# Optimization experiments

Measured on AMD Instinct MI355X. Metric: run time of the kernel, lower is better.

## Reference

```python
import jax, jax.numpy as jnp
import numpy as np

N_NODES = 100000
N_EDGES = 3200000
N_GRAPHS = 1024
HID = 64


def setup_inputs() -> dict:
    key = jax.random.key(0)
    ks = jax.random.split(key, 10)
    x = jax.random.normal(ks[0], (N_NODES, 5), dtype=jnp.float32)
    edge_index = jax.random.randint(ks[1], (2, N_EDGES), 0, N_NODES, dtype=jnp.int64)
    batch = jnp.sort(jax.random.randint(ks[2], (N_NODES,), 0, N_GRAPHS, dtype=jnp.int64))
    s = 0.1
    return {
        "x": x,
        "edge_index": edge_index,
        "batch": batch,
        "W1a": jax.random.normal(ks[3], (5, HID), dtype=jnp.float32) * s,
        "b1a": jnp.zeros((HID,), jnp.float32),
        "W1b": jax.random.normal(ks[4], (HID, HID), dtype=jnp.float32) * s,
        "b1b": jnp.zeros((HID,), jnp.float32),
        "W2a": jax.random.normal(ks[5], (HID, HID), dtype=jnp.float32) * s,
        "b2a": jnp.zeros((HID,), jnp.float32),
        "W2b": jax.random.normal(ks[6], (HID, HID), dtype=jnp.float32) * s,
        "b2b": jnp.zeros((HID,), jnp.float32),
        "Wc": jax.random.normal(ks[7], (HID, 2), dtype=jnp.float32) * s,
        "bc": jnp.zeros((2,), jnp.float32),
    }


def _gin_conv(h, src, dst, Wa, ba, Wb, bb):
    # GINConv (eps=0): mlp(h + sum of neighbor messages), messages flow src -> dst
    agg = jax.ops.segment_sum(h[src], dst, num_segments=N_NODES)
    z = h + agg
    return jax.nn.relu(z @ Wa + ba) @ Wb + bb


def reference(x, edge_index, batch, W1a, b1a, W1b, b1b, W2a, b2a, W2b, b2b, Wc, bc):
    src, dst = edge_index[0], edge_index[1]
    h = jax.nn.relu(_gin_conv(x, src, dst, W1a, b1a, W1b, b1b))
    h = jax.nn.relu(_gin_conv(h, src, dst, W2a, b2a, W2b, b2b))
    # global_mean_pool over graphs
    sums = jax.ops.segment_sum(h, batch, num_segments=N_GRAPHS)        # [G, H]
    counts = jax.ops.segment_sum(jnp.ones((N_NODES, 1), h.dtype), batch,
                                 num_segments=N_GRAPHS)                 # [G, 1]
    pooled = sums / jnp.maximum(counts, 1.0)
    return pooled @ Wc + bc
```

## Files before the change

### kernel.cpp

```cpp
#include <hip/hip_runtime.h>

#define N_NODES   100000
#define N_EDGES   3200000
#define N_GRAPHS  1024
#define HID       64

#define NPB   128
#define NB    782
#define NBLK  512
#define EPB   (N_EDGES / NBLK)
#define CAP   6144

using bf16x8 = __attribute__((ext_vector_type(8))) short;
using f32x4  = __attribute__((ext_vector_type(4))) float;
using f16x4  = __attribute__((ext_vector_type(4))) _Float16;


__global__ void __launch_bounds__(512) k_p1(const int* __restrict__ dst,
                                            int* __restrict__ cnt) {
    __shared__ int h[NB];
    for (int i = threadIdx.x; i < NB; i += 512) h[i] = 0;
    __syncthreads();
    int base = blockIdx.x * EPB;
    for (int i = threadIdx.x; i < EPB; i += 512)
        atomicAdd(&h[dst[base + i] >> 7], 1);
    __syncthreads();
    for (int i = threadIdx.x; i < NB; i += 512)
        cnt[blockIdx.x * NB + i] = h[i];
}

__global__ void __launch_bounds__(512) k_p2(const int* __restrict__ cnt,
                                            int* __restrict__ excT,
                                            int* __restrict__ btot) {
    __shared__ int wsum[8];
    int b = blockIdx.x, t = threadIdx.x;
    int v = cnt[t * NB + b];
    int incl = v;
#pragma unroll
    for (int off = 1; off < 64; off <<= 1) {
        int u = __shfl_up(incl, off, 64);
        if ((t & 63) >= off) incl += u;
    }
    if ((t & 63) == 63) wsum[t >> 6] = incl;
    __syncthreads();
    int woff = 0;
    for (int w = 0; w < (t >> 6); ++w) woff += wsum[w];
    excT[b * NBLK + t] = woff + incl - v;
    if (t == 511) btot[b] = woff + incl;
}

__global__ void __launch_bounds__(1024) k_p2b(const int* __restrict__ btot,
                                              int* __restrict__ bbase,
                                              int* __restrict__ rp) {
    __shared__ int s[1024];
    int t = threadIdx.x;
    int v = (t < NB) ? btot[t] : 0;
    s[t] = v;
    __syncthreads();
    for (int off = 1; off < 1024; off <<= 1) {
        int u = (t >= off) ? s[t - off] : 0;
        __syncthreads();
        s[t] += u;
        __syncthreads();
    }
    if (t < NB) bbase[t] = s[t] - v;
    if (t == 0) { bbase[NB] = N_EDGES; rp[N_NODES] = N_EDGES; }
}

__global__ void __launch_bounds__(512) k_p3(const int* __restrict__ src,
                                            const int* __restrict__ dst,
                                            const int* __restrict__ excT,
                                            const int* __restrict__ bbase,
                                            unsigned int* __restrict__ packed) {
    __shared__ int cur[NB];
    int blk = blockIdx.x;
    for (int i = threadIdx.x; i < NB; i += 512)
        cur[i] = bbase[i] + excT[i * NBLK + blk];
    __syncthreads();
    int base = blk * EPB;
    for (int i = threadIdx.x; i < EPB; i += 512) {
        int d = dst[base + i];
        int pos = atomicAdd(&cur[d >> 7], 1);
        packed[pos] = ((unsigned)(d & 127) << 17) | (unsigned)src[base + i];
    }
}

__global__ void __launch_bounds__(512) k_p4(const unsigned int* __restrict__ packed,
                                            const int* __restrict__ bbase,
                                            int* __restrict__ rp,
                                            int* __restrict__ srcs) {
    __shared__ int hist[NPB + 1];
    __shared__ int stage[CAP];
    int b = blockIdx.x, t = threadIdx.x;
    int lo = bbase[b], hi = bbase[b + 1];
    int n_e = hi - lo;
    if (t < NPB + 1) hist[t] = 0;
    __syncthreads();
    for (int i = t; i < n_e; i += 512)
        atomicAdd(&hist[(packed[lo + i] >> 17) + 1], 1);
    __syncthreads();
    for (int off = 1; off < NPB + 1; off <<= 1) {
        int u = 0;
        if (t < NPB + 1 && t >= off) u = hist[t - off];
        __syncthreads();
        if (t < NPB + 1 && t >= off) hist[t] += u;
        __syncthreads();
    }
    int nbase = b * NPB;
    if (t < NPB && nbase + t < N_NODES) rp[nbase + t] = lo + hist[t];
    __syncthreads();
    if (n_e <= CAP) {
        for (int i = t; i < n_e; i += 512) {
            unsigned v = packed[lo + i];
            int pos = atomicAdd(&hist[v >> 17], 1);
            stage[pos] = (int)(v & 0x1FFFFu);
        }
        __syncthreads();
        for (int i = t; i < n_e; i += 512) srcs[lo + i] = stage[i];
    } else {
        for (int i = t; i < n_e; i += 512) {
            unsigned v = packed[lo + i];
            int pos = atomicAdd(&hist[v >> 17], 1);
            srcs[lo + pos] = (int)(v & 0x1FFFFu);
        }
    }
}


__global__ void __launch_bounds__(256) k_padb(
    const float* __restrict__ x, float* __restrict__ x8,
    const int* __restrict__ batch, int* __restrict__ gstart,
    int* __restrict__ gend) {
    int i = blockIdx.x * 256 + threadIdx.x;
    if (i < N_NODES * 8) {
        int n = i >> 3, j = i & 7;
        x8[i] = (j < 5) ? x[n * 5 + j] : 0.f;
    }
    if (i < N_NODES) {
        int g = batch[i];
        if (i == 0 || batch[i - 1] != g) atomicMin(&gstart[g], i);
        if (i == N_NODES - 1 || batch[i + 1] != g) atomicMax(&gend[g], i + 1);
    }
}


__global__ void k_wconv3(const float* __restrict__ Wa, const float* __restrict__ Wb,
                         const float* __restrict__ Wc_,
                         unsigned short* __restrict__ pa, unsigned short* __restrict__ pb,
                         unsigned short* __restrict__ pc) {
    int which = blockIdx.x >> 4;
    const float* W = (which == 0) ? Wa : (which == 1) ? Wb : Wc_;
    unsigned short* pack = (which == 0) ? pa : (which == 1) ? pb : pc;
    int i = (blockIdx.x & 15) * 256 + threadIdx.x;
    if (i >= 4096) return;
    int j    = i & 7;
    int lane = (i >> 3) & 63;
    int t    = (i >> 9) & 3;
    int ks   = (i >> 11) & 1;
    int k   = ks * 32 + (lane >> 4) * 8 + j;
    int col = t * 16 + (lane & 15);
    float w = W[k * HID + col];
    unsigned b = __float_as_uint(w);
    unsigned short hiw = (unsigned short)(b >> 16);
    float lf = w - __uint_as_float(b & 0xFFFF0000u);
    unsigned short low = (unsigned short)(__float_as_uint(lf) >> 16);
    pack[(((ks * 4 + t)) * 64 + lane) * 8 + j]   = hiw;
    pack[((8 + ks * 4 + t) * 64 + lane) * 8 + j] = low;
}

__device__ __forceinline__ void split8(const float* v, bf16x8& hi, bf16x8& lo) {
#pragma unroll
    for (int j = 0; j < 8; ++j) {
        unsigned b = __float_as_uint(v[j]);
        hi[j] = (short)(b >> 16);
        float lf = v[j] - __uint_as_float(b & 0xFFFF0000u);
        lo[j] = (short)(__float_as_uint(lf) >> 16);
    }
}


__global__ void __launch_bounds__(512) k_g1(
    const float* __restrict__ x8, const int* __restrict__ rp,
    const int* __restrict__ srcs, const float* __restrict__ W1a,
    const float* __restrict__ b1a, float* __restrict__ t1) {
    __shared__ float sWa[5 * HID];
    __shared__ float sba[HID];
    for (int i = threadIdx.x; i < 5 * HID; i += 512) sWa[i] = W1a[i];
    if (threadIdx.x < HID) sba[threadIdx.x] = b1a[threadIdx.x];
    __syncthreads();

    int wave = (blockIdx.x * 512 + threadIdx.x) >> 6;
    int lane = threadIdx.x & 63;
    int grp = lane >> 4, fq = lane & 15;
    int half = fq >> 3, f = fq & 7;
    int n = wave * 4 + grp;
    int e0 = rp[n], e1 = rp[n + 1];

    float a = 0.f;
    int e = e0;
    for (; e + 8 <= e1; e += 8) {
        int i0 = e + half;
        int s0 = srcs[i0], s1 = srcs[i0 + 2], s2 = srcs[i0 + 4], s3 = srcs[i0 + 6];
        float v0 = x8[(size_t)s0 * 8 + f];
        float v1 = x8[(size_t)s1 * 8 + f];
        float v2 = x8[(size_t)s2 * 8 + f];
        float v3 = x8[(size_t)s3 * 8 + f];
        a += (v0 + v1) + (v2 + v3);
    }
    for (; e < e1; e += 2) {
        int i = e + half;
        if (i < e1) a += x8[(size_t)srcs[i] * 8 + f];
    }
    a += __shfl_xor(a, 8, 16);

    float zf[5];
#pragma unroll
    for (int ff = 0; ff < 5; ++ff)
        zf[ff] = __shfl(a, ff, 16) + x8[(size_t)n * 8 + ff];

    float4 t = *reinterpret_cast<const float4*>(&sba[fq * 4]);
#pragma unroll
    for (int ff = 0; ff < 5; ++ff) {
        const float4 w = *reinterpret_cast<const float4*>(&sWa[ff * HID + fq * 4]);
        t.x += zf[ff] * w.x; t.y += zf[ff] * w.y;
        t.z += zf[ff] * w.z; t.w += zf[ff] * w.w;
    }
    t.x = fmaxf(t.x, 0.f); t.y = fmaxf(t.y, 0.f);
    t.z = fmaxf(t.z, 0.f); t.w = fmaxf(t.w, 0.f);
    *reinterpret_cast<float4*>(t1 + (size_t)n * HID + fq * 4) = t;
}


__global__ void __launch_bounds__(256) k_mm1(
    const float* __restrict__ t1, const unsigned short* __restrict__ packB,
    const float* __restrict__ bias, _Float16* __restrict__ h1h) {
    int wave = threadIdx.x >> 6, lane = threadIdx.x & 63;
    int q = lane >> 4;
    int n0 = blockIdx.x * 64 + wave * 16;
    int arow = n0 + (lane & 15);
    if (arow >= N_NODES) arow = N_NODES - 1;
    const float* ar = t1 + (size_t)arow * HID + q * 8;
    alignas(16) float a0[8], a1[8];
    *reinterpret_cast<float4*>(a0)     = *reinterpret_cast<const float4*>(ar);
    *reinterpret_cast<float4*>(a0 + 4) = *reinterpret_cast<const float4*>(ar + 4);
    *reinterpret_cast<float4*>(a1)     = *reinterpret_cast<const float4*>(ar + 32);
    *reinterpret_cast<float4*>(a1 + 4) = *reinterpret_cast<const float4*>(ar + 36);
    bf16x8 Ah0, Al0, Ah1, Al1;
    split8(a0, Ah0, Al0);
    split8(a1, Ah1, Al1);
    const bf16x8* bp = reinterpret_cast<const bf16x8*>(packB);
#pragma unroll
    for (int t = 0; t < 4; ++t) {
        bf16x8 Bh0 = bp[(t) * 64 + lane];
        bf16x8 Bh1 = bp[(4 + t) * 64 + lane];
        bf16x8 Bl0 = bp[(8 + t) * 64 + lane];
        bf16x8 Bl1 = bp[(12 + t) * 64 + lane];
        f32x4 acc = {0.f, 0.f, 0.f, 0.f};
        acc = __builtin_amdgcn_mfma_f32_16x16x32_bf16(Ah0, Bh0, acc, 0, 0, 0);
        acc = __builtin_amdgcn_mfma_f32_16x16x32_bf16(Ah1, Bh1, acc, 0, 0, 0);
        acc = __builtin_amdgcn_mfma_f32_16x16x32_bf16(Al0, Bh0, acc, 0, 0, 0);
        acc = __builtin_amdgcn_mfma_f32_16x16x32_bf16(Al1, Bh1, acc, 0, 0, 0);
        acc = __builtin_amdgcn_mfma_f32_16x16x32_bf16(Ah0, Bl0, acc, 0, 0, 0);
        acc = __builtin_amdgcn_mfma_f32_16x16x32_bf16(Ah1, Bl1, acc, 0, 0, 0);
        acc = __builtin_amdgcn_mfma_f32_16x16x32_bf16(Al0, Bl0, acc, 0, 0, 0);
        acc = __builtin_amdgcn_mfma_f32_16x16x32_bf16(Al1, Bl1, acc, 0, 0, 0);
        int col = (lane & 15) + 16 * t;
        float bv = bias[col];
#pragma unroll
        for (int r = 0; r < 4; ++r) {
            int node = n0 + q * 4 + r;
            if (node < N_NODES)
                h1h[(size_t)node * HID + col] = (_Float16)fmaxf(acc[r] + bv, 0.f);
        }
    }
}


__device__ __forceinline__ void acc4(float4& z, f16x4 r) {
    z.x += (float)r.x; z.y += (float)r.y; z.z += (float)r.z; z.w += (float)r.w;
}

__global__ void __launch_bounds__(512) k_g2(
    const _Float16* __restrict__ h1h, const int* __restrict__ rp,
    const int* __restrict__ srcs, float* __restrict__ z2) {
    int wave = (blockIdx.x * 512 + threadIdx.x) >> 6;
    int lane = threadIdx.x & 63;
    int grp = lane >> 4, fq = lane & 15;
    int n = wave * 4 + grp;
    int e0 = rp[n], e1 = rp[n + 1];

    const f16x4* __restrict__ H = reinterpret_cast<const f16x4*>(h1h);
    f16x4 rs = H[(size_t)n * 16 + fq];
    float4 z = {(float)rs.x, (float)rs.y, (float)rs.z, (float)rs.w};

    int e = e0;
    for (; e + 8 <= e1; e += 8) {
        int s0 = srcs[e],     s1 = srcs[e + 1], s2 = srcs[e + 2], s3 = srcs[e + 3];
        int s4 = srcs[e + 4], s5 = srcs[e + 5], s6 = srcs[e + 6], s7 = srcs[e + 7];
        f16x4 v0 = H[(size_t)s0 * 16 + fq];
        f16x4 v1 = H[(size_t)s1 * 16 + fq];
        f16x4 v2 = H[(size_t)s2 * 16 + fq];
        f16x4 v3 = H[(size_t)s3 * 16 + fq];
        f16x4 v4 = H[(size_t)s4 * 16 + fq];
        f16x4 v5 = H[(size_t)s5 * 16 + fq];
        f16x4 v6 = H[(size_t)s6 * 16 + fq];
        f16x4 v7 = H[(size_t)s7 * 16 + fq];
        acc4(z, v0); acc4(z, v1); acc4(z, v2); acc4(z, v3);
        acc4(z, v4); acc4(z, v5); acc4(z, v6); acc4(z, v7);
    }
    for (; e < e1; ++e) {
        f16x4 v = H[(size_t)srcs[e] * 16 + fq];
        acc4(z, v);
    }
    *reinterpret_cast<float4*>(z2 + (size_t)n * HID + fq * 4) = z;
}


__global__ void __launch_bounds__(256) k_mm2(
    const float* __restrict__ z2, const unsigned short* __restrict__ packA,
    const unsigned short* __restrict__ packB, const float* __restrict__ b2a,
    const float* __restrict__ b2b, float* __restrict__ u_out) {
    __shared__ __align__(16) float tm[4][16][68];
    int wave = threadIdx.x >> 6, lane = threadIdx.x & 63;
    int q = lane >> 4;
    int n0 = blockIdx.x * 64 + wave * 16;
    int arow = n0 + (lane & 15);
    if (arow >= N_NODES) arow = N_NODES - 1;

    {
        const float* ar = z2 + (size_t)arow * HID + q * 8;
        alignas(16) float a0[8], a1[8];
        *reinterpret_cast<float4*>(a0)     = *reinterpret_cast<const float4*>(ar);
        *reinterpret_cast<float4*>(a0 + 4) = *reinterpret_cast<const float4*>(ar + 4);
        *reinterpret_cast<float4*>(a1)     = *reinterpret_cast<const float4*>(ar + 32);
        *reinterpret_cast<float4*>(a1 + 4) = *reinterpret_cast<const float4*>(ar + 36);
        bf16x8 Ah0, Al0, Ah1, Al1;
        split8(a0, Ah0, Al0);
        split8(a1, Ah1, Al1);
        const bf16x8* bp = reinterpret_cast<const bf16x8*>(packA);
#pragma unroll
        for (int t = 0; t < 4; ++t) {
            bf16x8 Bh0 = bp[(t) * 64 + lane];
            bf16x8 Bh1 = bp[(4 + t) * 64 + lane];
            bf16x8 Bl0 = bp[(8 + t) * 64 + lane];
            bf16x8 Bl1 = bp[(12 + t) * 64 + lane];
            f32x4 acc = {0.f, 0.f, 0.f, 0.f};
            acc = __builtin_amdgcn_mfma_f32_16x16x32_bf16(Ah0, Bh0, acc, 0, 0, 0);
            acc = __builtin_amdgcn_mfma_f32_16x16x32_bf16(Ah1, Bh1, acc, 0, 0, 0);
            acc = __builtin_amdgcn_mfma_f32_16x16x32_bf16(Al0, Bh0, acc, 0, 0, 0);
            acc = __builtin_amdgcn_mfma_f32_16x16x32_bf16(Al1, Bh1, acc, 0, 0, 0);
            acc = __builtin_amdgcn_mfma_f32_16x16x32_bf16(Ah0, Bl0, acc, 0, 0, 0);
            acc = __builtin_amdgcn_mfma_f32_16x16x32_bf16(Ah1, Bl1, acc, 0, 0, 0);
            acc = __builtin_amdgcn_mfma_f32_16x16x32_bf16(Al0, Bl0, acc, 0, 0, 0);
            acc = __builtin_amdgcn_mfma_f32_16x16x32_bf16(Al1, Bl1, acc, 0, 0, 0);
            int col = (lane & 15) + 16 * t;
            float bv = b2a[col];
#pragma unroll
            for (int r = 0; r < 4; ++r)
                tm[wave][q * 4 + r][col] = fmaxf(acc[r] + bv, 0.f);
        }
    }

    const float* tr = &tm[wave][lane & 15][0];
    alignas(16) float c0[8], c1[8];
    *reinterpret_cast<float4*>(c0)     = *reinterpret_cast<const float4*>(tr + q * 8);
    *reinterpret_cast<float4*>(c0 + 4) = *reinterpret_cast<const float4*>(tr + q * 8 + 4);
    *reinterpret_cast<float4*>(c1)     = *reinterpret_cast<const float4*>(tr + 32 + q * 8);
    *reinterpret_cast<float4*>(c1 + 4) = *reinterpret_cast<const float4*>(tr + 36 + q * 8);
    bf16x8 Ch0, Cl0, Ch1, Cl1;
    split8(c0, Ch0, Cl0);
    split8(c1, Ch1, Cl1);

    const bf16x8* bp = reinterpret_cast<const bf16x8*>(packB);
#pragma unroll
    for (int t = 0; t < 4; ++t) {
        bf16x8 Bh0 = bp[(t) * 64 + lane];
        bf16x8 Bh1 = bp[(4 + t) * 64 + lane];
        bf16x8 Bl0 = bp[(8 + t) * 64 + lane];
        bf16x8 Bl1 = bp[(12 + t) * 64 + lane];
        f32x4 acc = {0.f, 0.f, 0.f, 0.f};
        acc = __builtin_amdgcn_mfma_f32_16x16x32_bf16(Ch0, Bh0, acc, 0, 0, 0);
        acc = __builtin_amdgcn_mfma_f32_16x16x32_bf16(Ch1, Bh1, acc, 0, 0, 0);
        acc = __builtin_amdgcn_mfma_f32_16x16x32_bf16(Cl0, Bh0, acc, 0, 0, 0);
        acc = __builtin_amdgcn_mfma_f32_16x16x32_bf16(Cl1, Bh1, acc, 0, 0, 0);
        acc = __builtin_amdgcn_mfma_f32_16x16x32_bf16(Ch0, Bl0, acc, 0, 0, 0);
        acc = __builtin_amdgcn_mfma_f32_16x16x32_bf16(Ch1, Bl1, acc, 0, 0, 0);
        acc = __builtin_amdgcn_mfma_f32_16x16x32_bf16(Cl0, Bl0, acc, 0, 0, 0);
        acc = __builtin_amdgcn_mfma_f32_16x16x32_bf16(Cl1, Bl1, acc, 0, 0, 0);
        int col = (lane & 15) + 16 * t;
        float bv = b2b[col];
#pragma unroll
        for (int r = 0; r < 4; ++r) {
            int node = n0 + q * 4 + r;
            if (node < N_NODES)
                u_out[(size_t)node * HID + col] = fmaxf(acc[r] + bv, 0.f);
        }
    }
}


__global__ void __launch_bounds__(256) k_final2(
    const float* __restrict__ u, const int* __restrict__ gstart,
    const int* __restrict__ gend, const float* __restrict__ Wc,
    const float* __restrict__ bc, float* __restrict__ out) {
    __shared__ float red[4][64];
    int g = blockIdx.x, t = threadIdx.x;
    int col = t & 63, ch = t >> 6;
    int s = gstart[g], e = gend[g];
    float acc = 0.f;
    for (int i = s + ch; i < e; i += 4)
        acc += u[(size_t)i * HID + col];
    red[ch][col] = acc;
    __syncthreads();
    if (t < 64) {
        float p = red[0][t] + red[1][t] + red[2][t] + red[3][t];
        float count = (float)(e - s);
        p /= fmaxf(count, 1.0f);
        float r0 = p * Wc[t * 2 + 0];
        float r1 = p * Wc[t * 2 + 1];
#pragma unroll
        for (int m = 1; m < 64; m <<= 1) {
            r0 += __shfl_xor(r0, m, 64);
            r1 += __shfl_xor(r1, m, 64);
        }
        if (t == 0) {
            out[g * 2 + 0] = r0 + bc[0];
            out[g * 2 + 1] = r1 + bc[1];
        }
    }
}


extern "C" void kernel_launch(void* const* d_in, const int* in_sizes, int n_in,
                              void* d_out, int out_size, void* d_ws, size_t ws_size,
                              hipStream_t stream) {
    const float* x   = (const float*)d_in[0];
    const int* ei    = (const int*)d_in[1];
    const int* batch = (const int*)d_in[2];
    const float* W1a = (const float*)d_in[3];
    const float* b1a = (const float*)d_in[4];
    const float* W1b = (const float*)d_in[5];
    const float* b1b = (const float*)d_in[6];
    const float* W2a = (const float*)d_in[7];
    const float* b2a = (const float*)d_in[8];
    const float* W2b = (const float*)d_in[9];
    const float* b2b = (const float*)d_in[10];
    const float* Wc  = (const float*)d_in[11];
    const float* bc  = (const float*)d_in[12];
    float* out = (float*)d_out;

    const int* src = ei;
    const int* dst = ei + N_EDGES;

    char* ws = (char*)d_ws;
    size_t off = 0;
    auto alloc = [&](size_t bytes) {
        char* p = ws + off;
        off += (bytes + 127) & ~size_t(127);
        return p;
    };
    int*   rp    = (int*)alloc((N_NODES + 1) * sizeof(int));
    int*   srcs  = (int*)alloc((size_t)N_EDGES * sizeof(int));
    _Float16* h1h = (_Float16*)alloc((size_t)N_NODES * HID * sizeof(_Float16));
    float* t1    = (float*)alloc((size_t)N_NODES * HID * sizeof(float));
    float* z2    = (float*)alloc((size_t)N_NODES * HID * sizeof(float));
    float* x8    = (float*)alloc((size_t)N_NODES * 8 * sizeof(float));
    int*   btot  = (int*)alloc(NB * sizeof(int));
    int*   bbase = (int*)alloc((NB + 1) * sizeof(int));
    int*   gstart= (int*)alloc(N_GRAPHS * sizeof(int));
    int*   gend  = (int*)alloc(N_GRAPHS * sizeof(int));
    unsigned short* pk1b = (unsigned short*)alloc(8192 * sizeof(unsigned short));
    unsigned short* pk2a = (unsigned short*)alloc(8192 * sizeof(unsigned short));
    unsigned short* pk2b = (unsigned short*)alloc(8192 * sizeof(unsigned short));

    int* bcnt = (int*)t1;
    int* excT = (int*)t1 + NBLK * NB;
    unsigned int* packed = (unsigned int*)z2;

    hipMemsetAsync(gstart, 0x7F, N_GRAPHS * sizeof(int), stream);
    hipMemsetAsync(gend, 0, N_GRAPHS * sizeof(int), stream);

    k_p1 <<<NBLK, 512, 0, stream>>>(dst, bcnt);
    k_padb<<<(N_NODES * 8) / 256, 256, 0, stream>>>(x, x8, batch, gstart, gend);
    k_wconv3<<<48, 256, 0, stream>>>(W1b, W2a, W2b, pk1b, pk2a, pk2b);
    k_p2 <<<NB, 512, 0, stream>>>(bcnt, excT, btot);
    k_p2b<<<1, 1024, 0, stream>>>(btot, bbase, rp);
    k_p3 <<<NBLK, 512, 0, stream>>>(src, dst, excT, bbase, packed);
    k_p4 <<<NB, 512, 0, stream>>>(packed, bbase, rp, srcs);

    int gblocks = N_NODES / 32;
    int mblocks = (N_NODES + 63) / 64;

    k_g1 <<<gblocks, 512, 0, stream>>>(x8, rp, srcs, W1a, b1a, t1);
    k_mm1<<<mblocks, 256, 0, stream>>>(t1, pk1b, b1b, h1h);
    k_g2 <<<gblocks, 512, 0, stream>>>(h1h, rp, srcs, z2);
    k_mm2<<<mblocks, 256, 0, stream>>>(z2, pk2a, pk2b, b2a, b2b, t1);

    k_final2<<<N_GRAPHS, 256, 0, stream>>>(t1, gstart, gend, Wc, bc, out);
}
```

Baseline: 290.3 us.

## Do local per-block bucket sort in shared memory and gather segments in CSR pass

The edge bucketing pass now sorts each block's edges locally in shared memory by destination bucket and writes them out contiguously, instead of scattering each edge to its global position. The per-bucket CSR pass then reads the matching segment from each of the 512 source blocks, using per-block local offsets and counts. The column scan kernel shrinks to a plain reduction. This swaps random global scatter writes for coalesced writes, at the cost of many short segmented reads in the CSR pass and extra shared-memory use (25 KB stage) in the bucketing kernel.

```diff
diff --git a/kernel.cpp b/kernel.cpp
--- a/kernel.cpp
+++ b/kernel.cpp
@@ -29,24 +29,21 @@
         cnt[blockIdx.x * NB + i] = h[i];
 }
 
-__global__ void __launch_bounds__(512) k_p2(const int* __restrict__ cnt,
-                                            int* __restrict__ excT,
-                                            int* __restrict__ btot) {
-    __shared__ int wsum[8];
+__global__ void __launch_bounds__(512) k_p2r(const int* __restrict__ cnt,
+                                             int* __restrict__ btot) {
+    __shared__ int ws[8];
     int b = blockIdx.x, t = threadIdx.x;
     int v = cnt[t * NB + b];
-    int incl = v;
-#pragma unroll
-    for (int off = 1; off < 64; off <<= 1) {
-        int u = __shfl_up(incl, off, 64);
-        if ((t & 63) >= off) incl += u;
-    }
-    if ((t & 63) == 63) wsum[t >> 6] = incl;
-    __syncthreads();
-    int woff = 0;
-    for (int w = 0; w < (t >> 6); ++w) woff += wsum[w];
-    excT[b * NBLK + t] = woff + incl - v;
-    if (t == 511) btot[b] = woff + incl;
+#pragma unroll
+    for (int m = 1; m < 64; m <<= 1) v += __shfl_xor(v, m, 64);
+    if ((t & 63) == 0) ws[t >> 6] = v;
+    __syncthreads();
+    if (t == 0) {
+        int s = 0;
+#pragma unroll
+        for (int w = 0; w < 8; ++w) s += ws[w];
+        btot[b] = s;
+    }
 }
 
 __global__ void __launch_bounds__(1024) k_p2b(const int* __restrict__ btot,
@@ -69,35 +66,63 @@
 
 __global__ void __launch_bounds__(512) k_p3(const int* __restrict__ src,
                                             const int* __restrict__ dst,
-                                            const int* __restrict__ excT,
-                                            const int* __restrict__ bbase,
+                                            const int* __restrict__ cnt,
+                                            int* __restrict__ locoff,
                                             unsigned int* __restrict__ packed) {
     __shared__ int cur[NB];
-    int blk = blockIdx.x;
-    for (int i = threadIdx.x; i < NB; i += 512)
-        cur[i] = bbase[i] + excT[i * NBLK + blk];
+    __shared__ unsigned int stage[EPB];
+    int blk = blockIdx.x, t = threadIdx.x;
+    for (int i = t; i < NB; i += 512)
+        cur[i] = (i == 0) ? 0 : cnt[blk * NB + i - 1];
+    __syncthreads();
+    for (int off = 1; off < NB; off <<= 1) {
+        int i0 = t, i1 = t + 512;
+        int v0 = (i0 < NB && i0 >= off) ? cur[i0 - off] : 0;
+        int v1 = (i1 < NB && i1 >= off) ? cur[i1 - off] : 0;
+        __syncthreads();
+        if (i0 < NB && i0 >= off) cur[i0] += v0;
+        if (i1 < NB && i1 >= off) cur[i1] += v1;
+        __syncthreads();
+    }
+    for (int i = t; i < NB; i += 512) locoff[blk * NB + i] = cur[i];
     __syncthreads();
     int base = blk * EPB;
-    for (int i = threadIdx.x; i < EPB; i += 512) {
+    for (int i = t; i < EPB; i += 512) {
         int d = dst[base + i];
         int pos = atomicAdd(&cur[d >> 7], 1);
-        packed[pos] = ((unsigned)(d & 127) << 17) | (unsigned)src[base + i];
-    }
+        stage[pos] = ((unsigned)(d & 127) << 17) | (unsigned)src[base + i];
+    }
+    __syncthreads();
+    for (int i = t; i < EPB; i += 512)
+        packed[base + i] = stage[i];
 }
 
 __global__ void __launch_bounds__(512) k_p4(const unsigned int* __restrict__ packed,
+                                            const int* __restrict__ locoff,
+                                            const int* __restrict__ cnt,
+                                            const int* __restrict__ btot,
                                             const int* __restrict__ bbase,
                                             int* __restrict__ rp,
                                             int* __restrict__ srcs) {
     __shared__ int hist[NPB + 1];
     __shared__ int stage[CAP];
+    __shared__ int segbase[NBLK];
+    __shared__ short seglen[NBLK];
     int b = blockIdx.x, t = threadIdx.x;
-    int lo = bbase[b], hi = bbase[b + 1];
-    int n_e = hi - lo;
+    int lo = bbase[b];
+    int n_e = btot[b];
+    if (t < NBLK) {
+        segbase[t] = t * EPB + locoff[t * NB + b];
+        seglen[t] = (short)cnt[t * NB + b];
+    }
     if (t < NPB + 1) hist[t] = 0;
     __syncthreads();
-    for (int i = t; i < n_e; i += 512)
-        atomicAdd(&hist[(packed[lo + i] >> 17) + 1], 1);
+    int g = t >> 4, f = t & 15;
+    for (int sb = g; sb < NBLK; sb += 32) {
+        int s0 = segbase[sb], sl = seglen[sb];
+        for (int i = f; i < sl; i += 16)
+            atomicAdd(&hist[(packed[s0 + i] >> 17) + 1], 1);
+    }
     __syncthreads();
     for (int off = 1; off < NPB + 1; off <<= 1) {
         int u = 0;
@@ -110,18 +135,24 @@
     if (t < NPB && nbase + t < N_NODES) rp[nbase + t] = lo + hist[t];
     __syncthreads();
     if (n_e <= CAP) {
-        for (int i = t; i < n_e; i += 512) {
-            unsigned v = packed[lo + i];
-            int pos = atomicAdd(&hist[v >> 17], 1);
-            stage[pos] = (int)(v & 0x1FFFFu);
+        for (int sb = g; sb < NBLK; sb += 32) {
+            int s0 = segbase[sb], sl = seglen[sb];
+            for (int i = f; i < sl; i += 16) {
+                unsigned v = packed[s0 + i];
+                int pos = atomicAdd(&hist[v >> 17], 1);
+                stage[pos] = (int)(v & 0x1FFFFu);
+            }
         }
         __syncthreads();
         for (int i = t; i < n_e; i += 512) srcs[lo + i] = stage[i];
     } else {
-        for (int i = t; i < n_e; i += 512) {
-            unsigned v = packed[lo + i];
-            int pos = atomicAdd(&hist[v >> 17], 1);
-            srcs[lo + pos] = (int)(v & 0x1FFFFu);
+        for (int sb = g; sb < NBLK; sb += 32) {
+            int s0 = segbase[sb], sl = seglen[sb];
+            for (int i = f; i < sl; i += 16) {
+                unsigned v = packed[s0 + i];
+                int pos = atomicAdd(&hist[v >> 17], 1);
+                srcs[lo + pos] = (int)(v & 0x1FFFFu);
+            }
         }
     }
 }
@@ -473,8 +504,8 @@
     unsigned short* pk2a = (unsigned short*)alloc(8192 * sizeof(unsigned short));
     unsigned short* pk2b = (unsigned short*)alloc(8192 * sizeof(unsigned short));
 
-    int* bcnt = (int*)t1;
-    int* excT = (int*)t1 + NBLK * NB;
+    int* bcnt   = (int*)t1;
+    int* locoff = (int*)t1 + NBLK * NB;
     unsigned int* packed = (unsigned int*)z2;
 
     hipMemsetAsync(gstart, 0x7F, N_GRAPHS * sizeof(int), stream);
@@ -483,10 +514,10 @@
     k_p1 <<<NBLK, 512, 0, stream>>>(dst, bcnt);
     k_padb<<<(N_NODES * 8) / 256, 256, 0, stream>>>(x, x8, batch, gstart, gend);
     k_wconv3<<<48, 256, 0, stream>>>(W1b, W2a, W2b, pk1b, pk2a, pk2b);
-    k_p2 <<<NB, 512, 0, stream>>>(bcnt, excT, btot);
+    k_p2r<<<NB, 512, 0, stream>>>(bcnt, btot);
     k_p2b<<<1, 1024, 0, stream>>>(btot, bbase, rp);
-    k_p3 <<<NBLK, 512, 0, stream>>>(src, dst, excT, bbase, packed);
-    k_p4 <<<NB, 512, 0, stream>>>(packed, bbase, rp, srcs);
+    k_p3 <<<NBLK, 512, 0, stream>>>(src, dst, bcnt, locoff, packed);
+    k_p4 <<<NB, 512, 0, stream>>>(packed, locoff, bcnt, btot, bbase, rp, srcs);
 
     int gblocks = N_NODES / 32;
     int mblocks = (N_NODES + 63) / 64;
```

Result: faster. 280.4 us (-3.4%).
